# Performance work log

Measured on AMD Instinct MI355X. Metric: run time of the kernel, lower is better.

## Reference

```python
import jax, jax.numpy as jnp
import numpy as np

N = 50000      # nodes
E = 800000     # edges (avg degree 16)
IN = 256       # in_features
HD = 4         # num_heads
D = 64         # out_features per head


def setup_inputs() -> dict:
    key = jax.random.key(0)
    k1, k2, k3, k4, k5 = jax.random.split(key, 5)
    h = jax.random.normal(k1, (N, IN), dtype=jnp.float32)
    edge_index = jax.random.randint(k2, (2, E), 0, N)
    # W stored as [in_features, num_heads*out_features] (h @ W == Linear(h))
    W = jax.random.normal(k3, (IN, HD * D), dtype=jnp.float32) * (1.0 / np.sqrt(IN))
    a_src = jax.random.normal(k4, (HD, D), dtype=jnp.float32) * 0.1
    a_dst = jax.random.normal(k5, (HD, D), dtype=jnp.float32) * 0.1
    return {"h": h, "edge_index": edge_index, "W": W, "a_src": a_src, "a_dst": a_dst}


def reference(h, edge_index, W, a_src, a_dst):
    n = h.shape[0]
    src, dst = edge_index[0], edge_index[1]
    # project: [N, H, D]
    hp = (h @ W).reshape(n, HD, D)
    # per-edge attention logits [E, H]
    e_src = jnp.einsum('ehd,hd->eh', hp[src], a_src)
    e_dst = jnp.einsum('ehd,hd->eh', hp[dst], a_dst)
    e = jax.nn.leaky_relu(e_src + e_dst, negative_slope=0.2)
    # segment softmax over incoming edges of each dst node
    e_max = jax.ops.segment_max(e, dst, num_segments=n)          # [N, H]
    ex = jnp.exp(e - e_max[dst])                                  # [E, H]
    e_sum = jax.ops.segment_sum(ex, dst, num_segments=n)         # [N, H]
    alpha = ex / (e_sum[dst] + 1e-16)                             # [E, H]
    # weighted aggregation
    msg = hp[src] * alpha[..., None]                              # [E, H, D]
    out = jax.ops.segment_sum(msg, dst, num_segments=n)          # [N, H, D]
    return out.reshape(n, HD * D)                                 # concat=True
```

## Files before the change

### kernel.cpp

```cpp
#include <hip/hip_runtime.h>

#define HD 4
#define D 64
#define NHD 256
#define N_IN 256

typedef __attribute__((ext_vector_type(8))) __bf16 bf16x8;
typedef __attribute__((ext_vector_type(4))) __bf16 bf16x4;
typedef __attribute__((ext_vector_type(4))) float f32x4;

constexpr int AROW = 40;

__global__ __launch_bounds__(256) void pre_kernel(const float* __restrict__ W,
                                                  __bf16* __restrict__ Wt,
                                                  const int* __restrict__ ei,
                                                  int* __restrict__ deg8, int Nn, int E) {
  const int b = blockIdx.x;
  if (b < N_IN) {
    const int k = b, n = threadIdx.x;
    Wt[n * N_IN + k] = (__bf16)W[k * NHD + n];
  } else {
    const int e = (b - N_IN) * 256 + threadIdx.x;
    const int c = b & 7;
    if (e < E) atomicAdd(&deg8[c * Nn + ei[E + e]], 1);
  }
}

__global__ __launch_bounds__(512) void gemm_scan_kernel(
    const float* __restrict__ A, const __bf16* __restrict__ Wt,
    const float* __restrict__ a_src, const float* __restrict__ a_dst,
    __bf16* __restrict__ hp16, float* __restrict__ s_out, float* __restrict__ t_out,
    int M, const int* __restrict__ deg8, int* __restrict__ partial,
    int* __restrict__ blocksum, int NB, int MT) {
  __shared__ __bf16 As[128 * AROW];
  __shared__ __bf16 Bs[256 * AROW];
  __shared__ int ws4[4];
  const int tid = threadIdx.x;

  if ((int)blockIdx.x < NB) {
    const int lane = tid & 63, wv = tid >> 6;
    const int base = blockIdx.x * 1024 + tid * 4;
    int v[4], sum = 0, incl = 0;
    if (tid < 256) {
#pragma unroll
      for (int j = 0; j < 4; ++j) {
        int n = base + j;
        int s = 0;
        if (n < M) {
#pragma unroll
          for (int c = 0; c < 8; ++c) s += deg8[c * M + n];
        }
        v[j] = s;
      }
      sum = v[0] + v[1] + v[2] + v[3];
      incl = sum;
#pragma unroll
      for (int off = 1; off < 64; off <<= 1) {
        int y = __shfl_up(incl, off);
        if (lane >= off) incl += y;
      }
      if (lane == 63) ws4[wv] = incl;
    }
    __syncthreads();
    if (tid < 256) {
      int wbase = 0;
#pragma unroll
      for (int w = 0; w < 4; ++w)
        if (w < wv) wbase += ws4[w];
      int excl = wbase + incl - sum;
      if (base + 0 < M) partial[base + 0] = excl;
      if (base + 1 < M) partial[base + 1] = excl + v[0];
      if (base + 2 < M) partial[base + 2] = excl + v[0] + v[1];
      if (base + 3 < M) partial[base + 3] = excl + v[0] + v[1] + v[2];
      if (tid == 255) blocksum[blockIdx.x] = wbase + incl;
    }
    return;
  }

  const int g = blockIdx.x - NB;
  const int lane = tid & 63, wv = tid >> 6;
  const int wr = wv >> 2, wc = wv & 3;
  const int c15 = lane & 15, quad = lane >> 4;
  const int m0 = g * 128;

  f32x4 acc[4][4];
#pragma unroll
  for (int i = 0; i < 4; ++i)
#pragma unroll
    for (int j = 0; j < 4; ++j) acc[i][j] = (f32x4){0.f, 0.f, 0.f, 0.f};

  const int am = tid >> 2, aks = (tid & 3) * 8;
  const int gr = m0 + am;
  const bool arow_ok = (gr < M);
  const float* Arow = &A[(size_t)gr * N_IN];
  const int bm = tid >> 1, bks = (tid & 1) * 16;
  const __bf16* Brow = &Wt[(size_t)bm * N_IN];

  for (int kc = 0; kc < 8; ++kc) {
    const int k0 = kc * 32;
    float4 f0, f1;
    if (arow_ok) {
      f0 = *(const float4*)&Arow[k0 + aks + 0];
      f1 = *(const float4*)&Arow[k0 + aks + 4];
    } else {
      f0 = f1 = make_float4(0.f, 0.f, 0.f, 0.f);
    }
    bf16x8 b0 = *(const bf16x8*)&Brow[k0 + bks];
    bf16x8 b1 = *(const bf16x8*)&Brow[k0 + bks + 8];

    __syncthreads();
    bf16x8 a0;
    a0[0] = (__bf16)f0.x; a0[1] = (__bf16)f0.y; a0[2] = (__bf16)f0.z; a0[3] = (__bf16)f0.w;
    a0[4] = (__bf16)f1.x; a0[5] = (__bf16)f1.y; a0[6] = (__bf16)f1.z; a0[7] = (__bf16)f1.w;
    *(bf16x8*)&As[am * AROW + aks] = a0;
    *(bf16x8*)&Bs[bm * AROW + bks] = b0;
    *(bf16x8*)&Bs[bm * AROW + bks + 8] = b1;
    __syncthreads();

    bf16x8 af[4], bf_[4];
#pragma unroll
    for (int i = 0; i < 4; ++i) {
      af[i]  = *(bf16x8*)&As[(wr * 64 + i * 16 + c15) * AROW + quad * 8];
      bf_[i] = *(bf16x8*)&Bs[(wc * 64 + i * 16 + c15) * AROW + quad * 8];
    }
#pragma unroll
    for (int mi = 0; mi < 4; ++mi)
#pragma unroll
      for (int ni = 0; ni < 4; ++ni)
        acc[mi][ni] = __builtin_amdgcn_mfma_f32_16x16x32_bf16(af[mi], bf_[ni], acc[mi][ni], 0, 0, 0);
  }

  const int head = wc;
  float av[4], ad[4];
#pragma unroll
  for (int ni = 0; ni < 4; ++ni) {
    av[ni] = a_src[head * D + ni * 16 + c15];
    ad[ni] = a_dst[head * D + ni * 16 + c15];
  }
  const int row0w = m0 + wr * 64;
#pragma unroll
  for (int mi = 0; mi < 4; ++mi) {
#pragma unroll
    for (int j = 0; j < 4; ++j) {
      float ps = acc[mi][0][j] * av[0] + acc[mi][1][j] * av[1] +
                 acc[mi][2][j] * av[2] + acc[mi][3][j] * av[3];
      float pt = acc[mi][0][j] * ad[0] + acc[mi][1][j] * ad[1] +
                 acc[mi][2][j] * ad[2] + acc[mi][3][j] * ad[3];
#pragma unroll
      for (int m = 1; m < 16; m <<= 1) {
        ps += __shfl_xor(ps, m);
        pt += __shfl_xor(pt, m);
      }
      const int row = row0w + mi * 16 + quad * 4 + j;
      if (c15 == 0 && row < M) {
        s_out[row * HD + head] = ps;
        t_out[row * HD + head] = pt;
      }
    }
#pragma unroll
    for (int ni = 0; ni < 4; ++ni) {
#pragma unroll
      for (int j = 0; j < 4; ++j) {
        const int row = row0w + mi * 16 + quad * 4 + j;
        const int col = wc * 64 + ni * 16 + c15;
        if (row < M) hp16[(size_t)row * NHD + col] = (__bf16)acc[mi][ni][j];
      }
    }
  }
}

__global__ __launch_bounds__(256) void scan23_kernel(const int* __restrict__ partial,
                                                     const int* __restrict__ blocksum,
                                                     const int* __restrict__ deg8,
                                                     int* __restrict__ row_ptr,
                                                     int* __restrict__ cursor8, int n, int NB) {
  __shared__ int s_off;
  const int tid = threadIdx.x;
  if (tid < 64) {
    int v = (tid < NB) ? blocksum[tid] : 0;
    int incl = v;
#pragma unroll
    for (int off = 1; off < 64; off <<= 1) {
      int y = __shfl_up(incl, off);
      if (tid >= off) incl += y;
    }
    int prev = __shfl_up(incl, 1);
    int excl = (tid == 0) ? 0 : prev;
    if (tid == (int)blockIdx.x) s_off = excl;
    if (blockIdx.x == 0 && tid == NB - 1) row_ptr[n] = incl;
  }
  __syncthreads();
  const int off = s_off;
  const int base = blockIdx.x * 1024 + tid * 4;
#pragma unroll
  for (int j = 0; j < 4; ++j) {
    const int node = base + j;
    if (node < n) {
      int rp = partial[node] + off;
      row_ptr[node] = rp;
      int run = rp;
#pragma unroll
      for (int c = 0; c < 8; ++c) {
        cursor8[c * n + node] = run;
        run += deg8[c * n + node];
      }
    }
  }
}

__global__ void scatter_kernel(const int* __restrict__ ei, int* __restrict__ cursor8,
                               int* __restrict__ csr_src, int Nn, int E) {
  int e = blockIdx.x * blockDim.x + threadIdx.x;
  if (e >= E) return;
  const int c = blockIdx.x & 7;
  int sn = ei[e], dn = ei[E + e];
  int pos = atomicAdd(&cursor8[c * Nn + dn], 1);
  csr_src[pos] = sn;
}

__global__ __launch_bounds__(256) void aggregate_kernel(
    const int* __restrict__ row_ptr, const int* __restrict__ csr_src,
    const float* __restrict__ s, const float* __restrict__ t,
    const __bf16* __restrict__ hp16, float* __restrict__ out, int N) {
  const int wave = threadIdx.x >> 6;
  const int lane = threadIdx.x & 63;
  const int node = blockIdx.x * 4 + wave;
  if (node >= N) return;
  const int h = lane >> 4;
  const int d0 = lane * 4;
  const int beg = row_ptr[node], end = row_ptr[node + 1];
  const float tn = t[node * HD + h];
  float num0 = 0.f, num1 = 0.f, num2 = 0.f, num3 = 0.f, den = 0.f;
  int i = beg;
  for (; i + 8 <= end; i += 8) {
    int sn[8];
#pragma unroll
    for (int u = 0; u < 8; ++u) sn[u] = csr_src[i + u];
    bf16x4 v[8];
#pragma unroll
    for (int u = 0; u < 8; ++u) v[u] = *(const bf16x4*)&hp16[(size_t)sn[u] * NHD + d0];
    float lg[8];
#pragma unroll
    for (int u = 0; u < 8; ++u) lg[u] = s[sn[u] * HD + h] + tn;
#pragma unroll
    for (int u = 0; u < 8; ++u) {
      lg[u] = fmaxf(lg[u], 0.2f * lg[u]);
      lg[u] = __expf(lg[u]);
    }
#pragma unroll
    for (int u = 0; u < 8; ++u) {
      den  += lg[u];
      num0 += lg[u] * (float)v[u][0];
      num1 += lg[u] * (float)v[u][1];
      num2 += lg[u] * (float)v[u][2];
      num3 += lg[u] * (float)v[u][3];
    }
  }
  for (; i + 4 <= end; i += 4) {
    int sn0 = csr_src[i], sn1 = csr_src[i + 1], sn2 = csr_src[i + 2], sn3 = csr_src[i + 3];
    bf16x4 v0 = *(const bf16x4*)&hp16[(size_t)sn0 * NHD + d0];
    bf16x4 v1 = *(const bf16x4*)&hp16[(size_t)sn1 * NHD + d0];
    bf16x4 v2 = *(const bf16x4*)&hp16[(size_t)sn2 * NHD + d0];
    bf16x4 v3 = *(const bf16x4*)&hp16[(size_t)sn3 * NHD + d0];
    float lg0 = s[sn0 * HD + h] + tn;
    float lg1 = s[sn1 * HD + h] + tn;
    float lg2 = s[sn2 * HD + h] + tn;
    float lg3 = s[sn3 * HD + h] + tn;
    lg0 = fmaxf(lg0, 0.2f * lg0);
    lg1 = fmaxf(lg1, 0.2f * lg1);
    lg2 = fmaxf(lg2, 0.2f * lg2);
    lg3 = fmaxf(lg3, 0.2f * lg3);
    float ex0 = __expf(lg0), ex1 = __expf(lg1), ex2 = __expf(lg2), ex3 = __expf(lg3);
    den += (ex0 + ex1) + (ex2 + ex3);
    num0 += ex0 * (float)v0[0] + ex1 * (float)v1[0] + ex2 * (float)v2[0] + ex3 * (float)v3[0];
    num1 += ex0 * (float)v0[1] + ex1 * (float)v1[1] + ex2 * (float)v2[1] + ex3 * (float)v3[1];
    num2 += ex0 * (float)v0[2] + ex1 * (float)v1[2] + ex2 * (float)v2[2] + ex3 * (float)v3[2];
    num3 += ex0 * (float)v0[3] + ex1 * (float)v1[3] + ex2 * (float)v2[3] + ex3 * (float)v3[3];
  }
  for (; i < end; ++i) {
    int sn0 = csr_src[i];
    bf16x4 v0 = *(const bf16x4*)&hp16[(size_t)sn0 * NHD + d0];
    float lg0 = s[sn0 * HD + h] + tn;
    lg0 = fmaxf(lg0, 0.2f * lg0);
    float ex0 = __expf(lg0);
    den += ex0;
    num0 += ex0 * (float)v0[0];
    num1 += ex0 * (float)v0[1];
    num2 += ex0 * (float)v0[2];
    num3 += ex0 * (float)v0[3];
  }
  const float inv = 1.0f / (den + 1e-16f);
  float4 o = make_float4(num0 * inv, num1 * inv, num2 * inv, num3 * inv);
  *(float4*)&out[(size_t)node * NHD + d0] = o;
}

extern "C" void kernel_launch(void* const* d_in, const int* in_sizes, int n_in,
                              void* d_out, int out_size, void* d_ws, size_t ws_size,
                              hipStream_t stream) {
  const float* h_ptr  = (const float*)d_in[0];
  const int*   ei     = (const int*)d_in[1];
  const float* W      = (const float*)d_in[2];
  const float* a_src  = (const float*)d_in[3];
  const float* a_dst  = (const float*)d_in[4];
  float* out = (float*)d_out;

  const int N = in_sizes[0] / N_IN;
  const int E = in_sizes[1] / 2;
  const int NB = (N + 1023) / 1024;
  const int MT = (N + 127) / 128;

  auto align256 = [](size_t x) { return (x + 255) & ~size_t(255); };
  char* base = (char*)d_ws;
  size_t off = 0;
  __bf16* hp16 = (__bf16*)(base + off);  off += align256((size_t)N * NHD * 2);
  __bf16* Wt   = (__bf16*)(base + off);  off += align256((size_t)N_IN * NHD * 2);
  float* s       = (float*)(base + off); off += align256((size_t)N * HD * 4);
  float* t       = (float*)(base + off); off += align256((size_t)N * HD * 4);
  int*   deg8    = (int*)(base + off);   off += align256((size_t)N * 8 * 4);
  int*   cursor8 = (int*)(base + off);   off += align256((size_t)N * 8 * 4);
  int*   partial = (int*)(base + off);   off += align256((size_t)N * 4);
  int*   blocksum= (int*)(base + off);   off += align256((size_t)NB * 4);
  int*   row_ptr = (int*)(base + off);   off += align256((size_t)(N + 1) * 4);
  int*   csr_src = (int*)(base + off);   off += align256((size_t)E * 4);

  hipMemsetAsync(deg8, 0, (size_t)N * 8 * 4, stream);
  pre_kernel<<<N_IN + (E + 255) / 256, 256, 0, stream>>>(W, Wt, ei, deg8, N, E);
  gemm_scan_kernel<<<NB + MT, 512, 0, stream>>>(h_ptr, Wt, a_src, a_dst,
                                                hp16, s, t, N, deg8, partial,
                                                blocksum, NB, MT);
  scan23_kernel<<<NB, 256, 0, stream>>>(partial, blocksum, deg8, row_ptr, cursor8, N, NB);
  scatter_kernel<<<(E + 255) / 256, 256, 0, stream>>>(ei, cursor8, csr_src, N, E);
  aggregate_kernel<<<(N + 3) / 4, 256, 0, stream>>>(row_ptr, csr_src, s, t, hp16, out, N);
}
```

Measured before the change: 275.1 us.

## Distribute edge index and softmax weights across lanes in GAT aggregation

In the aggregation kernel, each lane now loads one neighbor index per 16-edge chunk and computes one exp weight. Indices are broadcast with readlane and weights with shuffles, so the same index and exp are no longer recomputed by all 64 lanes. The next chunk's indices are prefetched, and the denominator is reduced with an xor-shuffle tree. This trades redundant loads and exp calls for cross-lane shuffle traffic and a more serial inner loop. The scatter kernel also gets explicit launch bounds.

Result: no change. 273.7 us (-0.5%).

```diff
diff --git a/kernel.cpp b/kernel.cpp
--- a/kernel.cpp
+++ b/kernel.cpp
@@ -208,8 +208,8 @@
   }
 }
 
-__global__ void scatter_kernel(const int* __restrict__ ei, int* __restrict__ cursor8,
-                               int* __restrict__ csr_src, int Nn, int E) {
+__global__ __launch_bounds__(256) void scatter_kernel(const int* __restrict__ ei, int* __restrict__ cursor8,
+                                                      int* __restrict__ csr_src, int Nn, int E) {
   int e = blockIdx.x * blockDim.x + threadIdx.x;
   if (e >= E) return;
   const int c = blockIdx.x & 7;
@@ -227,68 +227,58 @@
   const int node = blockIdx.x * 4 + wave;
   if (node >= N) return;
   const int h = lane >> 4;
+  const int j = lane & 15;
   const int d0 = lane * 4;
+  const int exbase = lane & 48;
   const int beg = row_ptr[node], end = row_ptr[node + 1];
   const float tn = t[node * HD + h];
   float num0 = 0.f, num1 = 0.f, num2 = 0.f, num3 = 0.f, den = 0.f;
+
   int i = beg;
-  for (; i + 8 <= end; i += 8) {
-    int sn[8];
-#pragma unroll
-    for (int u = 0; u < 8; ++u) sn[u] = csr_src[i + u];
-    bf16x4 v[8];
-#pragma unroll
-    for (int u = 0; u < 8; ++u) v[u] = *(const bf16x4*)&hp16[(size_t)sn[u] * NHD + d0];
-    float lg[8];
-#pragma unroll
-    for (int u = 0; u < 8; ++u) lg[u] = s[sn[u] * HD + h] + tn;
-#pragma unroll
-    for (int u = 0; u < 8; ++u) {
-      lg[u] = fmaxf(lg[u], 0.2f * lg[u]);
-      lg[u] = __expf(lg[u]);
-    }
-#pragma unroll
-    for (int u = 0; u < 8; ++u) {
-      den  += lg[u];
-      num0 += lg[u] * (float)v[u][0];
-      num1 += lg[u] * (float)v[u][1];
-      num2 += lg[u] * (float)v[u][2];
-      num3 += lg[u] * (float)v[u][3];
-    }
-  }
-  for (; i + 4 <= end; i += 4) {
-    int sn0 = csr_src[i], sn1 = csr_src[i + 1], sn2 = csr_src[i + 2], sn3 = csr_src[i + 3];
-    bf16x4 v0 = *(const bf16x4*)&hp16[(size_t)sn0 * NHD + d0];
-    bf16x4 v1 = *(const bf16x4*)&hp16[(size_t)sn1 * NHD + d0];
-    bf16x4 v2 = *(const bf16x4*)&hp16[(size_t)sn2 * NHD + d0];
-    bf16x4 v3 = *(const bf16x4*)&hp16[(size_t)sn3 * NHD + d0];
-    float lg0 = s[sn0 * HD + h] + tn;
-    float lg1 = s[sn1 * HD + h] + tn;
-    float lg2 = s[sn2 * HD + h] + tn;
-    float lg3 = s[sn3 * HD + h] + tn;
-    lg0 = fmaxf(lg0, 0.2f * lg0);
-    lg1 = fmaxf(lg1, 0.2f * lg1);
-    lg2 = fmaxf(lg2, 0.2f * lg2);
-    lg3 = fmaxf(lg3, 0.2f * lg3);
-    float ex0 = __expf(lg0), ex1 = __expf(lg1), ex2 = __expf(lg2), ex3 = __expf(lg3);
-    den += (ex0 + ex1) + (ex2 + ex3);
-    num0 += ex0 * (float)v0[0] + ex1 * (float)v1[0] + ex2 * (float)v2[0] + ex3 * (float)v3[0];
-    num1 += ex0 * (float)v0[1] + ex1 * (float)v1[1] + ex2 * (float)v2[1] + ex3 * (float)v3[1];
-    num2 += ex0 * (float)v0[2] + ex1 * (float)v1[2] + ex2 * (float)v2[2] + ex3 * (float)v3[2];
-    num3 += ex0 * (float)v0[3] + ex1 * (float)v1[3] + ex2 * (float)v2[3] + ex3 * (float)v3[3];
-  }
-  for (; i < end; ++i) {
-    int sn0 = csr_src[i];
-    bf16x4 v0 = *(const bf16x4*)&hp16[(size_t)sn0 * NHD + d0];
-    float lg0 = s[sn0 * HD + h] + tn;
-    lg0 = fmaxf(lg0, 0.2f * lg0);
-    float ex0 = __expf(lg0);
-    den += ex0;
-    num0 += ex0 * (float)v0[0];
-    num1 += ex0 * (float)v0[1];
-    num2 += ex0 * (float)v0[2];
-    num3 += ex0 * (float)v0[3];
-  }
+  if (i < end) {
+    int rem0 = end - i;
+    int sn_cur = csr_src[i + (j < rem0 ? j : rem0 - 1)];
+    while (i < end) {
+      const int rem = end - i;
+      const int cnt = rem < 16 ? rem : 16;
+      const int inext = i + 16;
+      int sn_next = 0;
+      if (inext < end) {
+        int rem2 = end - inext;
+        sn_next = csr_src[inext + (j < rem2 ? j : rem2 - 1)];
+      }
+      float lg = s[sn_cur * HD + h] + tn;
+      lg = fmaxf(lg, 0.2f * lg);
+      float ex = (j < rem) ? __expf(lg) : 0.f;
+      den += ex;
+      if (cnt == 16) {
+#pragma unroll
+        for (int u = 0; u < 16; ++u) {
+          const int snu = __builtin_amdgcn_readlane(sn_cur, u);
+          const float exu = __shfl(ex, exbase + u);
+          bf16x4 v = *(const bf16x4*)&hp16[(unsigned)snu * (unsigned)NHD + (unsigned)d0];
+          num0 += exu * (float)v[0];
+          num1 += exu * (float)v[1];
+          num2 += exu * (float)v[2];
+          num3 += exu * (float)v[3];
+        }
+      } else {
+        for (int u = 0; u < cnt; ++u) {
+          const int snu = __builtin_amdgcn_readlane(sn_cur, u);
+          const float exu = __shfl(ex, exbase + u);
+          bf16x4 v = *(const bf16x4*)&hp16[(unsigned)snu * (unsigned)NHD + (unsigned)d0];
+          num0 += exu * (float)v[0];
+          num1 += exu * (float)v[1];
+          num2 += exu * (float)v[2];
+          num3 += exu * (float)v[3];
+        }
+      }
+      sn_cur = sn_next;
+      i = inext;
+    }
+  }
+#pragma unroll
+  for (int m = 1; m < 16; m <<= 1) den += __shfl_xor(den, m);
   const float inv = 1.0f / (den + 1e-16f);
   float4 o = make_float4(num0 * inv, num1 * inv, num2 * inv, num3 * inv);
   *(float4*)&out[(size_t)node * NHD + d0] = o;
```
